# Kernel optimization log

Measured on AMD Instinct MI355X. Metric: run time of the kernel, lower is better.

## Reference

```python
import jax, jax.numpy as jnp
import numpy as np

N_HEAD = 16
W_SCALE = 0.02  # keep pre-softmax scores in a sane range


def setup_inputs() -> dict:
    key = jax.random.key(0)
    ks = jax.random.split(key, 9)
    B, T, C = 4, 2048, 1024
    x = jax.random.normal(ks[0], (B, T, C), dtype=jnp.float32)
    def w(k):
        return jax.random.normal(k, (C, C), dtype=jnp.float32) * W_SCALE
    return {
        "x": x,
        "Wq": w(ks[1]), "bq": jnp.zeros((C,), jnp.float32),
        "Wk": w(ks[2]), "bk": jnp.zeros((C,), jnp.float32),
        "Wv": w(ks[3]), "bv": jnp.zeros((C,), jnp.float32),
        "Wp": w(ks[4]), "bp": jnp.zeros((C,), jnp.float32),
    }


def reference(x, Wq, bq, Wk, bk, Wv, bv, Wp, bp):
    # Causal self-attention, prefill path (layer_past=None, use_cache=False),
    # dropout in eval mode (pdrop=0). Weights stored as [in, out]: y = x @ W + b.
    B, T, C = x.shape
    H = N_HEAD
    d = C // H
    # project and split heads: [B, H, T, d]
    def heads(W, b):
        return (jnp.einsum("btc,cd->btd", x, W) + b).reshape(B, T, H, d).transpose(0, 2, 1, 3)
    q = heads(Wq, bq)
    k = heads(Wk, bk)
    v = heads(Wv, bv)
    scale = 1.0 / jnp.sqrt(jnp.asarray(d, x.dtype))
    att = jnp.einsum("bhtd,bhsd->bhts", q, k) * scale  # [B, H, T, T]
    # causal mask: position t attends to s <= t
    causal = jnp.tril(jnp.ones((T, T), dtype=bool))
    att = jnp.where(causal[None, None, :, :], att, jnp.asarray(-jnp.inf, att.dtype))
    att = jax.nn.softmax(att, axis=-1)
    y = jnp.einsum("bhts,bhsd->bhtd", att, v)  # [B, H, T, d]
    y = y.transpose(0, 2, 1, 3).reshape(B, T, C)
    y = jnp.einsum("btc,cd->btd", y, Wp) + bp
    return y
```

## Files before the change

### kernel.cpp

```cpp
#include <hip/hip_runtime.h>

typedef unsigned short u16;
typedef __attribute__((ext_vector_type(8))) short bf16x8;
typedef __attribute__((ext_vector_type(4))) float f32x4;

__device__ __forceinline__ float bf2f(u16 h) {
    return __uint_as_float(((unsigned int)h) << 16);
}
__device__ __forceinline__ u16 f2bf(float f) {
    unsigned int u = __float_as_uint(f);
    u += 0x7FFFu + ((u >> 16) & 1u);
    return (u16)(u >> 16);
}

__device__ __forceinline__ void gl2lds16(const u16* g, u16* l) {
    __builtin_amdgcn_global_load_lds(
        (const __attribute__((address_space(1))) unsigned int*)g,
        (__attribute__((address_space(3))) unsigned int*)l,
        16, 0, 0);
}

__global__ void detect_dtype(const u16* __restrict__ x, int* __restrict__ flag) {
    __shared__ int cnt;
    if (threadIdx.x == 0) cnt = 0;
    __syncthreads();
    unsigned e = (x[2 * threadIdx.x] >> 7) & 0xFF;
    if (e >= 116 && e <= 132) atomicAdd(&cnt, 1);
    __syncthreads();
    if (threadIdx.x == 0) *flag = (cnt >= 96) ? 1 : 0;
}

__global__ __launch_bounds__(256) void convert_in(
    const void* __restrict__ in, u16* __restrict__ out, long n4,
    const int* __restrict__ flag)
{
    long i = (long)blockIdx.x * blockDim.x + threadIdx.x;
    if (i >= n4) return;
    if (*flag) {
        ((ushort4*)out)[i] = ((const ushort4*)in)[i];
    } else {
        float4 v = ((const float4*)in)[i];
        ushort4 r;
        r.x = f2bf(v.x); r.y = f2bf(v.y); r.z = f2bf(v.z); r.w = f2bf(v.w);
        ((ushort4*)out)[i] = r;
    }
}

__global__ __launch_bounds__(256) void transpose_conv(
    const void* __restrict__ in, u16* __restrict__ out, int R, int Cc,
    const int* __restrict__ flag)
{
    __shared__ u16 tile[32][33];
    int tx = threadIdx.x & 31, ty = threadIdx.x >> 5;
    int c0 = blockIdx.x * 32, r0 = blockIdx.y * 32;
    bool isbf = (*flag != 0);
#pragma unroll
    for (int g = 0; g < 4; ++g) {
        size_t idx = (size_t)(r0 + ty + g * 8) * Cc + c0 + tx;
        tile[ty + g * 8][tx] = isbf ? ((const u16*)in)[idx]
                                    : f2bf(((const float*)in)[idx]);
    }
    __syncthreads();
#pragma unroll
    for (int g = 0; g < 4; ++g)
        out[(size_t)(c0 + ty + g * 8) * R + r0 + tx] = tile[tx][ty + g * 8];
}

__global__ __launch_bounds__(256, 2) void gemm_qkv(
    const u16* __restrict__ A, const u16* __restrict__ Bt,
    const void* __restrict__ biasq, const void* __restrict__ biask,
    const void* __restrict__ biasv,
    u16* __restrict__ Qo, u16* __restrict__ Ko, u16* __restrict__ Vt,
    int M, int K, const int* __restrict__ flag)
{
    __shared__ __align__(16) u16 As[128 * 64];
    __shared__ __align__(16) u16 Bs[128 * 64];

    const int tid  = threadIdx.x;
    const int m0   = blockIdx.y * 128, n0 = blockIdx.x * 128;
    const int lane = tid & 63, wid = tid >> 6;
    const int wm   = (wid >> 1) * 64, wn = (wid & 1) * 64;
    const int m16  = lane & 15, quad = lane >> 4;
    const int isbf = *flag;

    const int srow   = wid * 8 + (lane >> 3);
    const int schunk = (lane & 7) * 8;

    f32x4 acc[4][4];
#pragma unroll
    for (int i = 0; i < 4; ++i)
#pragma unroll
        for (int j = 0; j < 4; ++j)
            acc[i][j] = (f32x4){0.f, 0.f, 0.f, 0.f};

    for (int k0 = 0; k0 < K; k0 += 64) {
#pragma unroll
        for (int g = 0; g < 4; ++g) {
            int r = g * 32 + srow;
            gl2lds16(&A[(size_t)(m0 + r) * K + k0 + schunk], &As[r * 64 + schunk]);
            gl2lds16(&Bt[(size_t)(n0 + r) * K + k0 + schunk], &Bs[r * 64 + schunk]);
        }
        __syncthreads();
#pragma unroll
        for (int ks = 0; ks < 64; ks += 32) {
            bf16x8 a[4], b[4];
#pragma unroll
            for (int i = 0; i < 4; ++i)
                a[i] = *(bf16x8*)&As[(wm + i * 16 + m16) * 64 + ks + quad * 8];
#pragma unroll
            for (int j = 0; j < 4; ++j)
                b[j] = *(bf16x8*)&Bs[(wn + j * 16 + m16) * 64 + ks + quad * 8];
#pragma unroll
            for (int i = 0; i < 4; ++i)
#pragma unroll
                for (int j = 0; j < 4; ++j)
                    acc[i][j] = __builtin_amdgcn_mfma_f32_16x16x32_bf16(
                        a[i], b[j], acc[i][j], 0, 0, 0);
        }
        __syncthreads();
    }

    const int region = n0 >> 10;
    const void* bias = (region == 0) ? biasq : (region == 1) ? biask : biasv;
    const int nbase = region << 10;

#pragma unroll
    for (int i = 0; i < 4; ++i) {
        int grow = m0 + wm + i * 16 + quad * 4;
#pragma unroll
        for (int j = 0; j < 4; ++j) {
            int gcol = n0 + wn + j * 16 + m16;
            int nl = gcol - nbase;
            float bv_ = isbf ? bf2f(((const u16*)bias)[nl])
                             : ((const float*)bias)[nl];
            if (region < 2) {
                u16* out = (region == 0) ? Qo : Ko;
#pragma unroll
                for (int r = 0; r < 4; ++r)
                    out[(size_t)(grow + r) * 1024 + nl] = f2bf(acc[i][j][r] + bv_);
            } else {
                int h = nl >> 6, dd = nl & 63;
                int bb = grow >> 11, s = grow & 2047;
                ushort4 pk;
                pk.x = f2bf(acc[i][j][0] + bv_);
                pk.y = f2bf(acc[i][j][1] + bv_);
                pk.z = f2bf(acc[i][j][2] + bv_);
                pk.w = f2bf(acc[i][j][3] + bv_);
                *(ushort4*)&Vt[(((size_t)bb * 16 + h) * 64 + dd) * 2048 + s] = pk;
            }
        }
    }
}

__global__ __launch_bounds__(256, 2) void gemm_bias(
    const u16* __restrict__ A, const u16* __restrict__ Bt,
    const void* __restrict__ bias, void* __restrict__ C,
    int M, int N, int K, int final_out, const int* __restrict__ flag)
{
    __shared__ __align__(16) u16 As[128 * 64];
    __shared__ __align__(16) u16 Bs[128 * 64];

    const int tid  = threadIdx.x;
    const int m0   = blockIdx.y * 128, n0 = blockIdx.x * 128;
    const int lane = tid & 63, wid = tid >> 6;
    const int wm   = (wid >> 1) * 64, wn = (wid & 1) * 64;
    const int m16  = lane & 15, quad = lane >> 4;
    const int isbf = *flag;

    const int srow   = wid * 8 + (lane >> 3);
    const int schunk = (lane & 7) * 8;

    f32x4 acc[4][4];
#pragma unroll
    for (int i = 0; i < 4; ++i)
#pragma unroll
        for (int j = 0; j < 4; ++j)
            acc[i][j] = (f32x4){0.f, 0.f, 0.f, 0.f};

    for (int k0 = 0; k0 < K; k0 += 64) {
#pragma unroll
        for (int g = 0; g < 4; ++g) {
            int r = g * 32 + srow;
            gl2lds16(&A[(size_t)(m0 + r) * K + k0 + schunk], &As[r * 64 + schunk]);
            gl2lds16(&Bt[(size_t)(n0 + r) * K + k0 + schunk], &Bs[r * 64 + schunk]);
        }
        __syncthreads();
#pragma unroll
        for (int ks = 0; ks < 64; ks += 32) {
            bf16x8 a[4], b[4];
#pragma unroll
            for (int i = 0; i < 4; ++i)
                a[i] = *(bf16x8*)&As[(wm + i * 16 + m16) * 64 + ks + quad * 8];
#pragma unroll
            for (int j = 0; j < 4; ++j)
                b[j] = *(bf16x8*)&Bs[(wn + j * 16 + m16) * 64 + ks + quad * 8];
#pragma unroll
            for (int i = 0; i < 4; ++i)
#pragma unroll
                for (int j = 0; j < 4; ++j)
                    acc[i][j] = __builtin_amdgcn_mfma_f32_16x16x32_bf16(
                        a[i], b[j], acc[i][j], 0, 0, 0);
        }
        __syncthreads();
    }

    const bool out_f32 = final_out && !isbf;
#pragma unroll
    for (int i = 0; i < 4; ++i) {
        int grow = m0 + wm + i * 16 + quad * 4;
#pragma unroll
        for (int j = 0; j < 4; ++j) {
            int gcol = n0 + wn + j * 16 + m16;
            float bv = isbf ? bf2f(((const u16*)bias)[gcol])
                            : ((const float*)bias)[gcol];
#pragma unroll
            for (int r = 0; r < 4; ++r) {
                float val = acc[i][j][r] + bv;
                size_t idx = (size_t)(grow + r) * N + gcol;
                if (out_f32) ((float*)C)[idx] = val;
                else         ((u16*)C)[idx]   = f2bf(val);
            }
        }
    }
}

__global__ __launch_bounds__(256, 2) void attn_flash(
    const u16* __restrict__ Q, const u16* __restrict__ Kb,
    const u16* __restrict__ Vt, u16* __restrict__ O, int T, int C)
{
    __shared__ __align__(16) u16 Ks[2][128 * 64];
    __shared__ __align__(16) u16 Vts[2][64 * 128];
    __shared__ __align__(16) u16 Ps[128 * 64];

    const int tid  = threadIdx.x;
    const int lane = tid & 63, wid = tid >> 6;
    const int m16  = lane & 15, quad = lane >> 4;
    const int sw   = m16 & 7;
    const int h = blockIdx.y, b = blockIdx.z;
    const float qscale = 0.125f * 1.44269504f;
    const float NEG = -3.0e4f;

    const size_t headoff = ((size_t)b * T) * C + h * 64;
    const size_t vthead  = ((size_t)(b * 16 + h) * 64) * T;
    const int ntiles = 2 * gridDim.x;

    for (int phase = 0; phase < 2; ++phase) {
        const int qt = phase ? (int)blockIdx.x : (ntiles - 1) - (int)blockIdx.x;

        if (phase) __syncthreads();

        bf16x8 aq[2][2];
#pragma unroll
        for (int i = 0; i < 2; ++i)
#pragma unroll
            for (int ks = 0; ks < 2; ++ks)
                aq[i][ks] = *(const bf16x8*)&Q[headoff +
                    (size_t)(qt * 128 + wid * 32 + i * 16 + m16) * C +
                    ks * 32 + quad * 8];

#pragma unroll
        for (int g = 0; g < 4; ++g) {
            int r  = g * 32 + wid * 8 + (lane >> 3);
            int cg = (lane & 7) ^ (r & 7);
            gl2lds16(&Kb[headoff + (size_t)r * C + cg * 8],
                     &Ks[0][r * 64 + (lane & 7) * 8]);
        }
#pragma unroll
        for (int g = 0; g < 4; ++g) {
            int r  = g * 16 + wid * 4 + (lane >> 4);
            int cg = (lane & 15) ^ (r & 7);
            gl2lds16(&Vt[vthead + (size_t)r * T + cg * 8],
                     &Vts[0][r * 128 + (lane & 15) * 8]);
        }

        float l_run[2] = {0.f, 0.f};
        f32x4 o_acc[2][4];
#pragma unroll
        for (int i = 0; i < 2; ++i)
#pragma unroll
            for (int n = 0; n < 4; ++n)
                o_acc[i][n] = (f32x4){0.f, 0.f, 0.f, 0.f};

        for (int st = 0; st <= qt; ++st) {
            __syncthreads();
            const int cur = st & 1;

            if (st < qt) {
                const int nxt = cur ^ 1;
#pragma unroll
                for (int g = 0; g < 4; ++g) {
                    int r  = g * 32 + wid * 8 + (lane >> 3);
                    int cg = (lane & 7) ^ (r & 7);
                    gl2lds16(&Kb[headoff + (size_t)((st + 1) * 128 + r) * C + cg * 8],
                             &Ks[nxt][r * 64 + (lane & 7) * 8]);
                }
#pragma unroll
                for (int g = 0; g < 4; ++g) {
                    int r  = g * 16 + wid * 4 + (lane >> 4);
                    int cg = (lane & 15) ^ (r & 7);
                    gl2lds16(&Vt[vthead + (size_t)r * T + (st + 1) * 128 + cg * 8],
                             &Vts[nxt][r * 128 + (lane & 15) * 8]);
                }
            }

            f32x4 sacc[2][8];
#pragma unroll
            for (int i = 0; i < 2; ++i)
#pragma unroll
                for (int j = 0; j < 8; ++j)
                    sacc[i][j] = (f32x4){0.f, 0.f, 0.f, 0.f};
#pragma unroll
            for (int ks = 0; ks < 2; ++ks) {
                bf16x8 bk[8];
#pragma unroll
                for (int j = 0; j < 8; ++j)
                    bk[j] = *(bf16x8*)&Ks[cur][(j * 16 + m16) * 64 +
                                              (((ks * 4 + quad) ^ sw) * 8)];
#pragma unroll
                for (int i = 0; i < 2; ++i)
#pragma unroll
                    for (int j = 0; j < 8; ++j)
                        sacc[i][j] = __builtin_amdgcn_mfma_f32_16x16x32_bf16(
                            bk[j], aq[i][ks], sacc[i][j], 0, 0, 0);
            }

            if (st == qt) {
#pragma unroll
                for (int i = 0; i < 2; ++i) {
                    const int q_in = wid * 32 + i * 16 + m16;
#pragma unroll
                    for (int j = 0; j < 8; ++j)
#pragma unroll
                        for (int r = 0; r < 4; ++r)
                            if ((j * 16 + quad * 4 + r) > q_in)
                                sacc[i][j][r] = NEG;
                }
            }

            float rs[2] = {0.f, 0.f};
#pragma unroll
            for (int half = 0; half < 2; ++half) {
#pragma unroll
                for (int i = 0; i < 2; ++i) {
#pragma unroll
                    for (int jh = 0; jh < 4; ++jh) {
                        int j = half * 4 + jh;
                        float p0 = exp2f(sacc[i][j][0] * qscale);
                        float p1 = exp2f(sacc[i][j][1] * qscale);
                        float p2 = exp2f(sacc[i][j][2] * qscale);
                        float p3 = exp2f(sacc[i][j][3] * qscale);
                        rs[i] += (p0 + p1) + (p2 + p3);
                        unsigned lo = ((__float_as_uint(p0) + 0x8000u) >> 16) |
                                      ((__float_as_uint(p1) + 0x8000u) & 0xFFFF0000u);
                        unsigned hi = ((__float_as_uint(p2) + 0x8000u) >> 16) |
                                      ((__float_as_uint(p3) + 0x8000u) & 0xFFFF0000u);
                        *(uint2*)&Ps[(wid * 32 + i * 16 + m16) * 64 +
                                     (((jh * 2 + (quad >> 1)) ^ sw) * 8) +
                                     (quad & 1) * 4] = make_uint2(lo, hi);
                    }
                }
#pragma unroll
                for (int k4l = 0; k4l < 2; ++k4l) {
                    int k4 = half * 2 + k4l;
                    bf16x8 ap[2], bv[4];
#pragma unroll
                    for (int i = 0; i < 2; ++i)
                        ap[i] = *(bf16x8*)&Ps[(wid * 32 + i * 16 + m16) * 64 +
                                              (((k4l * 4 + quad) ^ sw) * 8)];
#pragma unroll
                    for (int n = 0; n < 4; ++n)
                        bv[n] = *(bf16x8*)&Vts[cur][(n * 16 + m16) * 128 +
                                                   (((k4 * 4 + quad) ^ sw) * 8)];
#pragma unroll
                    for (int i = 0; i < 2; ++i)
#pragma unroll
                        for (int n = 0; n < 4; ++n)
                            o_acc[i][n] = __builtin_amdgcn_mfma_f32_16x16x32_bf16(
                                ap[i], bv[n], o_acc[i][n], 0, 0, 0);
                }
            }
            l_run[0] += rs[0];
            l_run[1] += rs[1];
        }

#pragma unroll
        for (int i = 0; i < 2; ++i) {
            l_run[i] += __shfl_xor(l_run[i], 16);
            l_run[i] += __shfl_xor(l_run[i], 32);
            float linv[4];
#pragma unroll
            for (int r = 0; r < 4; ++r)
                linv[r] = 1.f / __shfl(l_run[i], quad * 4 + r);
#pragma unroll
            for (int n = 0; n < 4; ++n) {
#pragma unroll
                for (int r = 0; r < 4; ++r) {
                    int tq = qt * 128 + wid * 32 + i * 16 + quad * 4 + r;
                    O[((size_t)b * T + tq) * C + h * 64 + n * 16 + m16] =
                        f2bf(o_acc[i][n][r] * linv[r]);
                }
            }
        }
    }
}

extern "C" void kernel_launch(void* const* d_in, const int* in_sizes, int n_in,
                              void* d_out, int out_size, void* d_ws, size_t ws_size,
                              hipStream_t stream)
{
    const void* x  = d_in[0];
    const void* Wq = d_in[1];
    const void* bq = d_in[2];
    const void* Wk = d_in[3];
    const void* bk = d_in[4];
    const void* Wv = d_in[5];
    const void* bv = d_in[6];
    const void* Wp = d_in[7];
    const void* bp = d_in[8];

    const int Bb = 4, T = 2048, C = 1024, H = 16;
    const int M = Bb * T, N = C, K = C;

    u16* wsp = (u16*)d_ws;
    const size_t WSZ = (size_t)C * C;
    const size_t MSZ = (size_t)M * C;
    u16* WtQKV = wsp;
    u16* WtP   = wsp + 3 * WSZ;
    u16* xb    = wsp + 4 * WSZ;
    u16* Qb    = xb + MSZ;
    u16* Kbf   = Qb + MSZ;
    u16* Vtb   = Kbf + MSZ;
    u16* tmp   = Vtb + MSZ;
    int* flag  = (int*)(tmp + MSZ);

    detect_dtype<<<1, 128, 0, stream>>>((const u16*)x, flag);
    convert_in<<<(int)(MSZ / 4 / 256), 256, 0, stream>>>(x, xb, MSZ / 4, flag);

    dim3 tb(256), tg(C / 32, C / 32);
    transpose_conv<<<tg, tb, 0, stream>>>(Wq, WtQKV,           C, C, flag);
    transpose_conv<<<tg, tb, 0, stream>>>(Wk, WtQKV + WSZ,     C, C, flag);
    transpose_conv<<<tg, tb, 0, stream>>>(Wv, WtQKV + 2 * WSZ, C, C, flag);
    transpose_conv<<<tg, tb, 0, stream>>>(Wp, WtP,             C, C, flag);

    dim3 qg(3 * N / 128, M / 128), qb(256);
    gemm_qkv<<<qg, qb, 0, stream>>>(xb, WtQKV, bq, bk, bv, Qb, Kbf, Vtb,
                                    M, K, flag);

    dim3 ag(T / 256, H, Bb), ab(256);
    attn_flash<<<ag, ab, 0, stream>>>(Qb, Kbf, Vtb, tmp, T, C);

    dim3 gg(N / 128, M / 128), gb(256);
    gemm_bias<<<gg, gb, 0, stream>>>(tmp, WtP, bp, d_out, M, N, K, 1, flag);
}
```

Measured before the change: 297.5 us.

## Shrink attention tiles to 64 queries with 2-wave blocks; fold softmax scale into Q

The flash attention kernel now uses 64-row query tiles and 64-key KV tiles with 128-thread blocks. The grid doubles and LDS per block shrinks, which aims to give more blocks per CU, better load balance across the causal triangle, and less wasted masked work on diagonal tiles. The softmax scale times log2(e) is folded into Q at the QKV GEMM epilogue, removing a multiply per score. In exchange there are more loop iterations and barriers per unit of work, and Q is rounded to bf16 after scaling.

Measured after the change: 301.3 us. Within noise of the previous version (+1.3%).

```diff
diff --git a/kernel.cpp b/kernel.cpp
--- a/kernel.cpp
+++ b/kernel.cpp
@@ -123,6 +123,7 @@
     const int region = n0 >> 10;
     const void* bias = (region == 0) ? biasq : (region == 1) ? biask : biasv;
     const int nbase = region << 10;
+    const float osc = (region == 0) ? (0.125f * 1.44269504f) : 1.0f;
 
 #pragma unroll
     for (int i = 0; i < 4; ++i) {
@@ -137,7 +138,8 @@
                 u16* out = (region == 0) ? Qo : Ko;
 #pragma unroll
                 for (int r = 0; r < 4; ++r)
-                    out[(size_t)(grow + r) * 1024 + nl] = f2bf(acc[i][j][r] + bv_);
+                    out[(size_t)(grow + r) * 1024 + nl] =
+                        f2bf((acc[i][j][r] + bv_) * osc);
             } else {
                 int h = nl >> 6, dd = nl & 63;
                 int bb = grow >> 11, s = grow & 2047;
@@ -224,29 +226,30 @@
     }
 }
 
-__global__ __launch_bounds__(256, 2) void attn_flash(
+__global__ __launch_bounds__(128, 2) void attn_flash(
     const u16* __restrict__ Q, const u16* __restrict__ Kb,
     const u16* __restrict__ Vt, u16* __restrict__ O, int T, int C)
 {
-    __shared__ __align__(16) u16 Ks[2][128 * 64];
-    __shared__ __align__(16) u16 Vts[2][64 * 128];
-    __shared__ __align__(16) u16 Ps[128 * 64];
+    __shared__ __align__(16) u16 Ks[2][64 * 64];
+    __shared__ __align__(16) u16 Vts[2][64 * 64];
+    __shared__ __align__(16) u16 Ps[64 * 64];
 
     const int tid  = threadIdx.x;
     const int lane = tid & 63, wid = tid >> 6;
     const int m16  = lane & 15, quad = lane >> 4;
     const int sw   = m16 & 7;
     const int h = blockIdx.y, b = blockIdx.z;
-    const float qscale = 0.125f * 1.44269504f;
     const float NEG = -3.0e4f;
 
     const size_t headoff = ((size_t)b * T) * C + h * 64;
     const size_t vthead  = ((size_t)(b * 16 + h) * 64) * T;
     const int ntiles = 2 * gridDim.x;
 
+    const int srow8 = tid >> 3;
+    const int sch   = tid & 7;
+
     for (int phase = 0; phase < 2; ++phase) {
         const int qt = phase ? (int)blockIdx.x : (ntiles - 1) - (int)blockIdx.x;
-
         if (phase) __syncthreads();
 
         bf16x8 aq[2][2];
@@ -255,22 +258,22 @@
 #pragma unroll
             for (int ks = 0; ks < 2; ++ks)
                 aq[i][ks] = *(const bf16x8*)&Q[headoff +
-                    (size_t)(qt * 128 + wid * 32 + i * 16 + m16) * C +
+                    (size_t)(qt * 64 + wid * 32 + i * 16 + m16) * C +
                     ks * 32 + quad * 8];
 
 #pragma unroll
         for (int g = 0; g < 4; ++g) {
-            int r  = g * 32 + wid * 8 + (lane >> 3);
-            int cg = (lane & 7) ^ (r & 7);
+            int r  = g * 16 + srow8;
+            int cg = sch ^ (r & 7);
             gl2lds16(&Kb[headoff + (size_t)r * C + cg * 8],
-                     &Ks[0][r * 64 + (lane & 7) * 8]);
+                     &Ks[0][r * 64 + sch * 8]);
         }
 #pragma unroll
         for (int g = 0; g < 4; ++g) {
-            int r  = g * 16 + wid * 4 + (lane >> 4);
-            int cg = (lane & 15) ^ (r & 7);
+            int r  = g * 16 + srow8;
+            int cg = sch ^ (r & 7);
             gl2lds16(&Vt[vthead + (size_t)r * T + cg * 8],
-                     &Vts[0][r * 128 + (lane & 15) * 8]);
+                     &Vts[0][r * 64 + sch * 8]);
         }
 
         float l_run[2] = {0.f, 0.f};
@@ -281,45 +284,46 @@
             for (int n = 0; n < 4; ++n)
                 o_acc[i][n] = (f32x4){0.f, 0.f, 0.f, 0.f};
 
-        for (int st = 0; st <= qt; ++st) {
+        const int nst = qt + 1;
+        for (int st = 0; st < nst; ++st) {
             __syncthreads();
             const int cur = st & 1;
 
-            if (st < qt) {
+            if (st + 1 < nst) {
                 const int nxt = cur ^ 1;
 #pragma unroll
                 for (int g = 0; g < 4; ++g) {
-                    int r  = g * 32 + wid * 8 + (lane >> 3);
-                    int cg = (lane & 7) ^ (r & 7);
-                    gl2lds16(&Kb[headoff + (size_t)((st + 1) * 128 + r) * C + cg * 8],
-                             &Ks[nxt][r * 64 + (lane & 7) * 8]);
+                    int r  = g * 16 + srow8;
+                    int cg = sch ^ (r & 7);
+                    gl2lds16(&Kb[headoff + (size_t)((st + 1) * 64 + r) * C + cg * 8],
+                             &Ks[nxt][r * 64 + sch * 8]);
                 }
 #pragma unroll
                 for (int g = 0; g < 4; ++g) {
-                    int r  = g * 16 + wid * 4 + (lane >> 4);
-                    int cg = (lane & 15) ^ (r & 7);
-                    gl2lds16(&Vt[vthead + (size_t)r * T + (st + 1) * 128 + cg * 8],
-                             &Vts[nxt][r * 128 + (lane & 15) * 8]);
+                    int r  = g * 16 + srow8;
+                    int cg = sch ^ (r & 7);
+                    gl2lds16(&Vt[vthead + (size_t)r * T + (st + 1) * 64 + cg * 8],
+                             &Vts[nxt][r * 64 + sch * 8]);
                 }
             }
 
-            f32x4 sacc[2][8];
+            f32x4 sacc[2][4];
 #pragma unroll
             for (int i = 0; i < 2; ++i)
 #pragma unroll
-                for (int j = 0; j < 8; ++j)
+                for (int j = 0; j < 4; ++j)
                     sacc[i][j] = (f32x4){0.f, 0.f, 0.f, 0.f};
 #pragma unroll
             for (int ks = 0; ks < 2; ++ks) {
-                bf16x8 bk[8];
-#pragma unroll
-                for (int j = 0; j < 8; ++j)
+                bf16x8 bk[4];
+#pragma unroll
+                for (int j = 0; j < 4; ++j)
                     bk[j] = *(bf16x8*)&Ks[cur][(j * 16 + m16) * 64 +
                                               (((ks * 4 + quad) ^ sw) * 8)];
 #pragma unroll
                 for (int i = 0; i < 2; ++i)
 #pragma unroll
-                    for (int j = 0; j < 8; ++j)
+                    for (int j = 0; j < 4; ++j)
                         sacc[i][j] = __builtin_amdgcn_mfma_f32_16x16x32_bf16(
                             bk[j], aq[i][ks], sacc[i][j], 0, 0, 0);
             }
@@ -329,7 +333,7 @@
                 for (int i = 0; i < 2; ++i) {
                     const int q_in = wid * 32 + i * 16 + m16;
 #pragma unroll
-                    for (int j = 0; j < 8; ++j)
+                    for (int j = 0; j < 4; ++j)
 #pragma unroll
                         for (int r = 0; r < 4; ++r)
                             if ((j * 16 + quad * 4 + r) > q_in)
@@ -339,45 +343,41 @@
 
             float rs[2] = {0.f, 0.f};
 #pragma unroll
-            for (int half = 0; half < 2; ++half) {
-#pragma unroll
-                for (int i = 0; i < 2; ++i) {
-#pragma unroll
-                    for (int jh = 0; jh < 4; ++jh) {
-                        int j = half * 4 + jh;
-                        float p0 = exp2f(sacc[i][j][0] * qscale);
-                        float p1 = exp2f(sacc[i][j][1] * qscale);
-                        float p2 = exp2f(sacc[i][j][2] * qscale);
-                        float p3 = exp2f(sacc[i][j][3] * qscale);
-                        rs[i] += (p0 + p1) + (p2 + p3);
-                        unsigned lo = ((__float_as_uint(p0) + 0x8000u) >> 16) |
-                                      ((__float_as_uint(p1) + 0x8000u) & 0xFFFF0000u);
-                        unsigned hi = ((__float_as_uint(p2) + 0x8000u) >> 16) |
-                                      ((__float_as_uint(p3) + 0x8000u) & 0xFFFF0000u);
-                        *(uint2*)&Ps[(wid * 32 + i * 16 + m16) * 64 +
-                                     (((jh * 2 + (quad >> 1)) ^ sw) * 8) +
-                                     (quad & 1) * 4] = make_uint2(lo, hi);
-                    }
+            for (int i = 0; i < 2; ++i) {
+#pragma unroll
+                for (int j = 0; j < 4; ++j) {
+                    float p0 = exp2f(sacc[i][j][0]);
+                    float p1 = exp2f(sacc[i][j][1]);
+                    float p2 = exp2f(sacc[i][j][2]);
+                    float p3 = exp2f(sacc[i][j][3]);
+                    rs[i] += (p0 + p1) + (p2 + p3);
+                    unsigned lo = ((__float_as_uint(p0) + 0x8000u) >> 16) |
+                                  ((__float_as_uint(p1) + 0x8000u) & 0xFFFF0000u);
+                    unsigned hi = ((__float_as_uint(p2) + 0x8000u) >> 16) |
+                                  ((__float_as_uint(p3) + 0x8000u) & 0xFFFF0000u);
+                    *(uint2*)&Ps[(wid * 32 + i * 16 + m16) * 64 +
+                                 (((j * 2 + (quad >> 1)) ^ sw) * 8) +
+                                 (quad & 1) * 4] = make_uint2(lo, hi);
                 }
-#pragma unroll
-                for (int k4l = 0; k4l < 2; ++k4l) {
-                    int k4 = half * 2 + k4l;
-                    bf16x8 ap[2], bv[4];
-#pragma unroll
-                    for (int i = 0; i < 2; ++i)
-                        ap[i] = *(bf16x8*)&Ps[(wid * 32 + i * 16 + m16) * 64 +
-                                              (((k4l * 4 + quad) ^ sw) * 8)];
+            }
+
+#pragma unroll
+            for (int k4 = 0; k4 < 2; ++k4) {
+                bf16x8 ap[2], bv[4];
+#pragma unroll
+                for (int i = 0; i < 2; ++i)
+                    ap[i] = *(bf16x8*)&Ps[(wid * 32 + i * 16 + m16) * 64 +
+                                          (((k4 * 4 + quad) ^ sw) * 8)];
+#pragma unroll
+                for (int n = 0; n < 4; ++n)
+                    bv[n] = *(bf16x8*)&Vts[cur][(n * 16 + m16) * 64 +
+                                               (((k4 * 4 + quad) ^ sw) * 8)];
+#pragma unroll
+                for (int i = 0; i < 2; ++i)
 #pragma unroll
                     for (int n = 0; n < 4; ++n)
-                        bv[n] = *(bf16x8*)&Vts[cur][(n * 16 + m16) * 128 +
-                                                   (((k4 * 4 + quad) ^ sw) * 8)];
-#pragma unroll
-                    for (int i = 0; i < 2; ++i)
-#pragma unroll
-                        for (int n = 0; n < 4; ++n)
-                            o_acc[i][n] = __builtin_amdgcn_mfma_f32_16x16x32_bf16(
-                                ap[i], bv[n], o_acc[i][n], 0, 0, 0);
-                }
+                        o_acc[i][n] = __builtin_amdgcn_mfma_f32_16x16x32_bf16(
+                            ap[i], bv[n], o_acc[i][n], 0, 0, 0);
             }
             l_run[0] += rs[0];
             l_run[1] += rs[1];
@@ -395,7 +395,7 @@
             for (int n = 0; n < 4; ++n) {
 #pragma unroll
                 for (int r = 0; r < 4; ++r) {
-                    int tq = qt * 128 + wid * 32 + i * 16 + quad * 4 + r;
+                    int tq = qt * 64 + wid * 32 + i * 16 + quad * 4 + r;
                     O[((size_t)b * T + tq) * C + h * 64 + n * 16 + m16] =
                         f2bf(o_acc[i][n][r] * linv[r]);
                 }
@@ -446,7 +446,7 @@
     gemm_qkv<<<qg, qb, 0, stream>>>(xb, WtQKV, bq, bk, bv, Qb, Kbf, Vtb,
                                     M, K, flag);
 
-    dim3 ag(T / 256, H, Bb), ab(256);
+    dim3 ag(T / 128, H, Bb), ab(128);
     attn_flash<<<ag, ab, 0, stream>>>(Qb, Kbf, Vtb, tmp, T, C);
 
     dim3 gg(N / 128, M / 128), gb(256);
```
